# Kernel optimization log

Measured on AMD Instinct MI355X. Metric: run time of the kernel, lower is better.

The kernel has to match this reference:

```python
import jax, jax.numpy as jnp
import numpy as np

EMBED = 768
NH = 12          # num_heads
NL = 3           # num_levels
NP = 4           # num_points
DV = 384         # value dim = embed_dim * deform_ratio(0.5)
DH = DV // NH    # per-head value dim = 32
B = 16
LQ = 1024        # (512/16)^2 ViT tokens
SHAPES = [(64, 64), (32, 32), (16, 16)]  # 1/8, 1/16, 1/32 pyramid of 512x512
LKV = sum(h * w for h, w in SHAPES)      # 5376
EPS = 1e-6


def layer_norm(x, w, b):
    mu = jnp.mean(x, axis=-1, keepdims=True)
    var = jnp.mean((x - mu) ** 2, axis=-1, keepdims=True)
    return (x - mu) / jnp.sqrt(var + EPS) * w + b


def bilinear_sample(v, loc, H, W):
    # v: (B, NH, H*W, DH); loc: (B, Lq, NH, P, 2) normalized in [0,1]
    # Matches torch grid_sample(align_corners=False, padding_mode='zeros').
    Bv, Lq = loc.shape[0], loc.shape[1]
    x = loc[..., 0] * W - 0.5
    y = loc[..., 1] * H - 0.5
    x0 = jnp.floor(x)
    y0 = jnp.floor(y)
    dx = x - x0
    dy = y - y0
    x0i = x0.astype(jnp.int32)
    y0i = y0.astype(jnp.int32)

    def gather(xi, yi):
        valid = (xi >= 0) & (xi < W) & (yi >= 0) & (yi < H)  # (B,Lq,NH,P)
        xc = jnp.clip(xi, 0, W - 1)
        yc = jnp.clip(yi, 0, H - 1)
        lin = (yc * W + xc).transpose(0, 2, 1, 3).reshape(Bv, NH, Lq * NP)
        g = jnp.take_along_axis(v, lin[..., None], axis=2)  # (B,NH,Lq*P,DH)
        g = g.reshape(Bv, NH, Lq, NP, DH).transpose(0, 2, 1, 3, 4)  # (B,Lq,NH,P,DH)
        return g * valid[..., None].astype(g.dtype)

    g00 = gather(x0i, y0i)
    g01 = gather(x0i + 1, y0i)
    g10 = gather(x0i, y0i + 1)
    g11 = gather(x0i + 1, y0i + 1)
    w00 = ((1 - dx) * (1 - dy))[..., None]
    w01 = (dx * (1 - dy))[..., None]
    w10 = ((1 - dx) * dy)[..., None]
    w11 = (dx * dy)[..., None]
    return g00 * w00 + g01 * w01 + g10 * w10 + g11 * w11


def ms_deform_attn_core(value, shapes_list, loc, aw):
    # value: (B,LKV,NH,DH); loc: (B,Lq,NH,NL,NP,2); aw: (B,Lq,NH,NL,NP)
    Bv, Lq = loc.shape[0], loc.shape[1]
    samples = []
    idx = 0
    for l, (H, W) in enumerate(shapes_list):
        v = value[:, idx:idx + H * W].transpose(0, 2, 1, 3)  # (B,NH,HW,DH)
        idx += H * W
        samples.append(bilinear_sample(v, loc[:, :, :, l], H, W))
    s = jnp.stack(samples, axis=3)  # (B,Lq,NH,NL,NP,DH)
    o = jnp.einsum('bqhlp,bqhlpd->bqhd', aw, s)
    return o.reshape(Bv, Lq, NH * DH)


def setup_inputs() -> dict:
    key = jax.random.key(0)
    ks = jax.random.split(key, 12)

    def n(k, shape, s=0.02):
        return jax.random.normal(k, shape, jnp.float32) * s

    return {
        'q': jax.random.normal(ks[0], (B, LQ, EMBED), jnp.float32),
        'reference_points': jax.random.uniform(ks[1], (B, LQ, NL, 2), jnp.float32),
        'kv': jax.random.normal(ks[2], (B, LKV, EMBED), jnp.float32),
        'spatial_shapes': jnp.asarray(SHAPES, jnp.int32),
        'level_start_index': jnp.asarray(
            np.cumsum([0] + [h * w for h, w in SHAPES])[:-1], jnp.int32),
        'ln1_w': jnp.ones(EMBED, jnp.float32),
        'ln1_b': jnp.zeros(EMBED, jnp.float32),
        'ln2_w': jnp.ones(EMBED, jnp.float32),
        'ln2_b': jnp.zeros(EMBED, jnp.float32),
        'gamma': n(ks[3], (EMBED,), 0.1),
        'w_off': n(ks[4], (EMBED, NH * NL * NP * 2)),
        'b_off': n(ks[5], (NH * NL * NP * 2,), 0.01),
        'w_aw': n(ks[6], (EMBED, NH * NL * NP)),
        'b_aw': jnp.zeros(NH * NL * NP, jnp.float32),
        'w_val': n(ks[7], (EMBED, DV)),
        'b_val': jnp.zeros(DV, jnp.float32),
        'w_out': n(ks[8], (DV, EMBED)),
        'b_out': jnp.zeros(EMBED, jnp.float32),
    }


def reference(q, reference_points, kv, spatial_shapes, level_start_index,
              ln1_w, ln1_b, ln2_w, ln2_b, gamma,
              w_off, b_off, w_aw, b_aw, w_val, b_val, w_out, b_out):
    shapes_list = [tuple(int(v) for v in r) for r in np.asarray(spatial_shapes)]
    Bq, Lq, _ = q.shape
    qn = layer_norm(q, ln1_w, ln1_b)
    kvn = layer_norm(kv, ln2_w, ln2_b)
    value = (kvn @ w_val + b_val).reshape(Bq, -1, NH, DH)
    off = (qn @ w_off + b_off).reshape(Bq, Lq, NH, NL, NP, 2)
    aw = (qn @ w_aw + b_aw).reshape(Bq, Lq, NH, NL * NP)
    aw = jax.nn.softmax(aw, axis=-1).reshape(Bq, Lq, NH, NL, NP)
    # offset normalizer is (W_l, H_l) per level
    wh = jnp.asarray([[w, h] for (h, w) in shapes_list], q.dtype)  # (NL,2)
    loc = reference_points[:, :, None, :, None, :] + off / wh[None, None, None, :, None, :]
    attn = ms_deform_attn_core(value, shapes_list, loc, aw)
    attn = attn @ w_out + b_out
    return q + gamma * attn
```

## Files before the change

### kernel.cpp

```cpp
#include <hip/hip_runtime.h>

#define DEV __device__ __forceinline__

typedef short bf16x8 __attribute__((ext_vector_type(8)));
typedef float f32x4 __attribute__((ext_vector_type(4)));
typedef unsigned int u32;
typedef __attribute__((address_space(1))) const u32* gas_ptr;
typedef __attribute__((address_space(3))) u32* las_ptr;

DEV short f2bf(float f) {
  union { float f; unsigned u; } un; un.f = f;
  unsigned r = un.u + 0x7FFFu + ((un.u >> 16) & 1u);
  return (short)(r >> 16);
}
DEV float bf2f(unsigned short s) {
  union { unsigned u; float f; } un;
  un.u = ((unsigned)s) << 16;
  return un.f;
}
DEV void gload16(const short* g, short* l) {
  __builtin_amdgcn_global_load_lds((gas_ptr)g, (las_ptr)l, 16, 0, 0);
}
DEV float hsum4(float4 v) { return v.x + v.y + v.z + v.w; }

__global__ __launch_bounds__(256) void pack_weights_kernel(
    const float* __restrict__ w_val, const float* __restrict__ w_off,
    const float* __restrict__ w_aw, const float* __restrict__ w_out,
    const float* __restrict__ b_off, const float* __restrict__ b_aw,
    short* __restrict__ wT_val, short* __restrict__ wT_offaw,
    short* __restrict__ wT_out, float* __restrict__ bias_cat) {
  int gid = blockIdx.x * 256 + threadIdx.x;
  const int S0 = 768 * 384, S1 = 768 * 288, S2 = 768 * 144, S3 = 384 * 768;
  const int S4 = 80 * 768, S5 = 512;
  if (gid < S0) { int k = gid / 384, n = gid % 384; wT_val[n * 768 + k] = f2bf(w_val[gid]); return; }
  gid -= S0;
  if (gid < S1) { int k = gid / 288, n = gid % 288; wT_offaw[n * 768 + k] = f2bf(w_off[gid]); return; }
  gid -= S1;
  if (gid < S2) { int k = gid / 144, n = gid % 144; wT_offaw[(288 + n) * 768 + k] = f2bf(w_aw[gid]); return; }
  gid -= S2;
  if (gid < S3) { int k = gid / 768, n = gid % 768; wT_out[n * 384 + k] = f2bf(w_out[gid]); return; }
  gid -= S3;
  if (gid < S4) { wT_offaw[432 * 768 + gid] = 0; return; }
  gid -= S4;
  if (gid < S5) { bias_cat[gid] = (gid < 288) ? b_off[gid] : (gid < 432 ? b_aw[gid - 288] : 0.f); }
}

__global__ __launch_bounds__(256) void ln_norm4_kernel(
    const float* __restrict__ x, const float* __restrict__ w,
    const float* __restrict__ b, short* __restrict__ y) {
  const int wv = threadIdx.x >> 6, lane = threadIdx.x & 63;
  const int row = blockIdx.x * 4 + wv;
  const float* xr = x + (size_t)row * 768;
  float4 v0 = *(const float4*)(xr + lane * 4);
  float4 v1 = *(const float4*)(xr + 256 + lane * 4);
  float4 v2 = *(const float4*)(xr + 512 + lane * 4);
  float s = hsum4(v0) + hsum4(v1) + hsum4(v2);
  #pragma unroll
  for (int off = 32; off > 0; off >>= 1) s += __shfl_xor(s, off, 64);
  const float mu = s * (1.f / 768.f);
  float4 d0 = make_float4(v0.x - mu, v0.y - mu, v0.z - mu, v0.w - mu);
  float4 d1 = make_float4(v1.x - mu, v1.y - mu, v1.z - mu, v1.w - mu);
  float4 d2 = make_float4(v2.x - mu, v2.y - mu, v2.z - mu, v2.w - mu);
  float vs = d0.x * d0.x + d0.y * d0.y + d0.z * d0.z + d0.w * d0.w +
             d1.x * d1.x + d1.y * d1.y + d1.z * d1.z + d1.w * d1.w +
             d2.x * d2.x + d2.y * d2.y + d2.z * d2.z + d2.w * d2.w;
  #pragma unroll
  for (int off = 32; off > 0; off >>= 1) vs += __shfl_xor(vs, off, 64);
  const float rs = rsqrtf(vs * (1.f / 768.f) + 1e-6f);
  const float4 w0 = *(const float4*)(w + lane * 4);
  const float4 w1 = *(const float4*)(w + 256 + lane * 4);
  const float4 w2 = *(const float4*)(w + 512 + lane * 4);
  const float4 b0 = *(const float4*)(b + lane * 4);
  const float4 b1 = *(const float4*)(b + 256 + lane * 4);
  const float4 b2 = *(const float4*)(b + 512 + lane * 4);
  unsigned short* yr = (unsigned short*)y + (size_t)row * 768;
  ushort4 o;
  o.x = (unsigned short)f2bf(d0.x * rs * w0.x + b0.x);
  o.y = (unsigned short)f2bf(d0.y * rs * w0.y + b0.y);
  o.z = (unsigned short)f2bf(d0.z * rs * w0.z + b0.z);
  o.w = (unsigned short)f2bf(d0.w * rs * w0.w + b0.w);
  *(ushort4*)(yr + lane * 4) = o;
  o.x = (unsigned short)f2bf(d1.x * rs * w1.x + b1.x);
  o.y = (unsigned short)f2bf(d1.y * rs * w1.y + b1.y);
  o.z = (unsigned short)f2bf(d1.z * rs * w1.z + b1.z);
  o.w = (unsigned short)f2bf(d1.w * rs * w1.w + b1.w);
  *(ushort4*)(yr + 256 + lane * 4) = o;
  o.x = (unsigned short)f2bf(d2.x * rs * w2.x + b2.x);
  o.y = (unsigned short)f2bf(d2.y * rs * w2.y + b2.y);
  o.z = (unsigned short)f2bf(d2.z * rs * w2.z + b2.z);
  o.w = (unsigned short)f2bf(d2.w * rs * w2.w + b2.w);
  *(ushort4*)(yr + 512 + lane * 4) = o;
}

template <int EMODE>
__global__ __launch_bounds__(256, 3) void gemm128_kernel(
    const short* __restrict__ A, const short* __restrict__ Wt,
    const float* __restrict__ bias, const float* __restrict__ qres,
    const float* __restrict__ gamma, void* __restrict__ Cout,
    const int N, const int K) {
  __shared__ __align__(16) short As[128 * 32];
  __shared__ __align__(16) short Bs[128 * 32];
  const int tid = threadIdx.x;
  const int wave = tid >> 6, lane = tid & 63;

  const int nx = gridDim.x;
  const int id = blockIdx.y * nx + blockIdx.x;
  const int cpx = (nx * gridDim.y) >> 3;
  const int swz = (id & 7) * cpx + (id >> 3);
  const int n0 = (swz % nx) * 128, row0 = (swz / nx) * 128;

  const int lr = lane & 15, quad = lane >> 4;
  const int wm = wave >> 1, wn = wave & 1;

  const short* gA[2]; const short* gB[2];
  #pragma unroll
  for (int rnd = 0; rnd < 2; rnd++) {
    int G = rnd * 256 + wave * 64 + lane;
    int line = G >> 3, pos = G & 7, x = pos ^ (line & 7);
    int r = line * 2 + (x >> 2), qk = (x & 3) * 8;
    gA[rnd] = A + (size_t)(row0 + r) * K + qk;
    gB[rnd] = Wt + (size_t)(n0 + r) * K + qk;
  }
  short* ldsA[2] = {&As[(wave * 64) * 8], &As[(256 + wave * 64) * 8]};
  short* ldsB[2] = {&Bs[(wave * 64) * 8], &Bs[(256 + wave * 64) * 8]};

  const short* aF[4]; const short* bF[4];
  #pragma unroll
  for (int t4 = 0; t4 < 4; t4++) {
    int r = wm * 64 + t4 * 16 + lr;
    int line = r >> 1, pos = ((r & 1) * 4 + quad) ^ (line & 7);
    aF[t4] = &As[(line * 8 + pos) * 8];
    int rb = wn * 64 + t4 * 16 + lr;
    int lineb = rb >> 1, posb = ((rb & 1) * 4 + quad) ^ (lineb & 7);
    bF[t4] = &Bs[(lineb * 8 + posb) * 8];
  }

  f32x4 acc[4][4];
  #pragma unroll
  for (int i = 0; i < 4; i++)
    #pragma unroll
    for (int j = 0; j < 4; j++)
      #pragma unroll
      for (int e = 0; e < 4; e++) acc[i][j][e] = 0.f;

  for (int k0 = 0; k0 < K; k0 += 32) {
    gload16(gA[0], ldsA[0]);
    gload16(gA[1], ldsA[1]);
    gload16(gB[0], ldsB[0]);
    gload16(gB[1], ldsB[1]);
    gA[0] += 32; gA[1] += 32; gB[0] += 32; gB[1] += 32;
    __syncthreads();
    bf16x8 av[4], bv[4];
    #pragma unroll
    for (int t4 = 0; t4 < 4; t4++) {
      av[t4] = *(const bf16x8*)aF[t4];
      bv[t4] = *(const bf16x8*)bF[t4];
    }
    #pragma unroll
    for (int ct = 0; ct < 4; ct++)
      #pragma unroll
      for (int rt = 0; rt < 4; rt++)
        acc[rt][ct] = __builtin_amdgcn_mfma_f32_16x16x32_bf16(av[rt], bv[ct], acc[rt][ct], 0, 0, 0);
    __syncthreads();
  }

  #pragma unroll
  for (int ct = 0; ct < 4; ct++) {
    const int n = n0 + wn * 64 + ct * 16 + lr;
    const float bs = bias[n];
    const float gm = (EMODE == 2) ? gamma[n] : 0.f;
    #pragma unroll
    for (int rt = 0; rt < 4; rt++) {
      #pragma unroll
      for (int i = 0; i < 4; i++) {
        const int m = row0 + wm * 64 + rt * 16 + quad * 4 + i;
        float v = acc[rt][ct][i] + bs;
        if (EMODE == 0) {
          ((short*)Cout)[(size_t)m * N + n] = f2bf(v);
        } else if (EMODE == 1) {
          ((float*)Cout)[(size_t)m * N + n] = v;
        } else {
          ((float*)Cout)[(size_t)m * N + n] = qres[(size_t)m * N + n] + gm * v;
        }
      }
    }
  }
}

__global__ __launch_bounds__(384) void sampler_kernel(
    const float* __restrict__ offaw,
    const float* __restrict__ refp,
    const short* __restrict__ value,
    short* __restrict__ o) {
  const int tid = threadIdx.x;
  const int qi = tid / 96, t = tid % 96;
  const int head = t >> 3, ln4 = t & 7;
  const int bq = blockIdx.x * 4 + qi;
  __shared__ __align__(16) float s[4][440];
  __shared__ float sref[4][6];
  const float* row = offaw + (size_t)bq * 512;
  #pragma unroll
  for (int i = t; i < 108; i += 96)
    *(float4*)&s[qi][i * 4] = *(const float4*)&row[i * 4];
  if (t < 6) sref[qi][t] = refp[(size_t)bq * 6 + t];
  __syncthreads();

  const float* awp = &s[qi][288 + head * 12];
  float mx = awp[0];
  #pragma unroll
  for (int j = 1; j < 12; j++) mx = fmaxf(mx, awp[j]);
  float wgt[12];
  float ssum = 0.f;
  #pragma unroll
  for (int j = 0; j < 12; j++) { float e = __expf(awp[j] - mx); wgt[j] = e; ssum += e; }
  const float inv = 1.f / ssum;

  const int b = bq >> 10;
  const unsigned short* vb =
      (const unsigned short*)value + (size_t)b * 5376 * 384 + head * 32 + ln4 * 4;
  float4 acc = make_float4(0.f, 0.f, 0.f, 0.f);
  const int HW[3] = {64, 32, 16};
  const int starts[3] = {0, 4096, 5120};
  #pragma unroll
  for (int l = 0; l < 3; l++) {
    const int Wi = HW[l];
    const float Wf = (float)Wi;
    const float rx = sref[qi][l * 2], ry = sref[qi][l * 2 + 1];
    const unsigned short* base = vb + (size_t)starts[l] * 384;
    #pragma unroll
    for (int p = 0; p < 4; p++) {
      const int oi = ((head * 3 + l) * 4 + p) * 2;
      float x = fmaf(rx, Wf, s[qi][oi] - 0.5f);
      float y = fmaf(ry, Wf, s[qi][oi + 1] - 0.5f);
      float xf = floorf(x), yf = floorf(y);
      float dx = x - xf, dy = y - yf;
      int x0 = (int)xf, y0 = (int)yf;
      int x1 = x0 + 1, y1 = y0 + 1;
      int x0c = min(max(x0, 0), Wi - 1), x1c = min(max(x1, 0), Wi - 1);
      int y0c = min(max(y0, 0), Wi - 1), y1c = min(max(y1, 0), Wi - 1);
      float wx0 = (x0 >= 0 && x0 < Wi) ? (1.f - dx) : 0.f;
      float wx1 = (x1 < Wi && x1 >= 0) ? dx : 0.f;
      float wy0 = (y0 >= 0 && y0 < Wi) ? (1.f - dy) : 0.f;
      float wy1 = (y1 < Wi && y1 >= 0) ? dy : 0.f;
      const ushort4 u00 = *(const ushort4*)(base + (size_t)(y0c * Wi + x0c) * 384);
      const ushort4 u01 = *(const ushort4*)(base + (size_t)(y0c * Wi + x1c) * 384);
      const ushort4 u10 = *(const ushort4*)(base + (size_t)(y1c * Wi + x0c) * 384);
      const ushort4 u11 = *(const ushort4*)(base + (size_t)(y1c * Wi + x1c) * 384);
      const float w00 = wx0 * wy0, w01 = wx1 * wy0, w10 = wx0 * wy1, w11 = wx1 * wy1;
      const float g = wgt[l * 4 + p];
      acc.x += g * (w00 * bf2f(u00.x) + w01 * bf2f(u01.x) + w10 * bf2f(u10.x) + w11 * bf2f(u11.x));
      acc.y += g * (w00 * bf2f(u00.y) + w01 * bf2f(u01.y) + w10 * bf2f(u10.y) + w11 * bf2f(u11.y));
      acc.z += g * (w00 * bf2f(u00.z) + w01 * bf2f(u01.z) + w10 * bf2f(u10.z) + w11 * bf2f(u11.z));
      acc.w += g * (w00 * bf2f(u00.w) + w01 * bf2f(u01.w) + w10 * bf2f(u10.w) + w11 * bf2f(u11.w));
    }
  }
  ushort4 outv;
  outv.x = (unsigned short)f2bf(acc.x * inv);
  outv.y = (unsigned short)f2bf(acc.y * inv);
  outv.z = (unsigned short)f2bf(acc.z * inv);
  outv.w = (unsigned short)f2bf(acc.w * inv);
  *(ushort4*)((unsigned short*)o + (size_t)bq * 384 + head * 32 + ln4 * 4) = outv;
}

extern "C" void kernel_launch(void* const* d_in, const int* in_sizes, int n_in,
                              void* d_out, int out_size, void* d_ws, size_t ws_size,
                              hipStream_t stream) {
  (void)in_sizes; (void)n_in; (void)out_size; (void)ws_size;
  const float* q     = (const float*)d_in[0];
  const float* refp  = (const float*)d_in[1];
  const float* kv    = (const float*)d_in[2];
  const float* ln1w  = (const float*)d_in[5];
  const float* ln1b  = (const float*)d_in[6];
  const float* ln2w  = (const float*)d_in[7];
  const float* ln2b  = (const float*)d_in[8];
  const float* gamma = (const float*)d_in[9];
  const float* w_off = (const float*)d_in[10];
  const float* b_off = (const float*)d_in[11];
  const float* w_aw  = (const float*)d_in[12];
  const float* b_aw  = (const float*)d_in[13];
  const float* w_val = (const float*)d_in[14];
  const float* b_val = (const float*)d_in[15];
  const float* w_out = (const float*)d_in[16];
  const float* b_out = (const float*)d_in[17];
  float* out = (float*)d_out;

  char* wsp = (char*)d_ws;
  size_t cur = 0;
  auto alloc = [&](size_t bytes) -> void* {
    cur = (cur + 255) & ~(size_t)255;
    void* p = wsp + cur;
    cur += bytes;
    return p;
  };
  short*  wT_val   = (short*)alloc((size_t)384 * 768 * 2);
  short*  wT_offaw = (short*)alloc((size_t)512 * 768 * 2);
  short*  wT_out   = (short*)alloc((size_t)768 * 384 * 2);
  float*  bias_cat = (float*)alloc((size_t)512 * 4);
  short*  kvn      = (short*)alloc((size_t)86016 * 768 * 2);
  short*  qn       = (short*)alloc((size_t)16384 * 768 * 2);
  short*  value    = (short*)alloc((size_t)86016 * 384 * 2);
  float*  offaw    = (float*)alloc((size_t)16384 * 512 * 4);
  short*  obuf     = (short*)alloc((size_t)16384 * 384 * 2);

  pack_weights_kernel<<<3842, 256, 0, stream>>>(w_val, w_off, w_aw, w_out, b_off,
                                                b_aw, wT_val, wT_offaw, wT_out,
                                                bias_cat);
  ln_norm4_kernel<<<21504, 256, 0, stream>>>(kv, ln2w, ln2b, kvn);
  ln_norm4_kernel<<<4096, 256, 0, stream>>>(q, ln1w, ln1b, qn);
  gemm128_kernel<0><<<dim3(3, 672), 256, 0, stream>>>(
      kvn, wT_val, b_val, nullptr, nullptr, value, 384, 768);
  gemm128_kernel<1><<<dim3(4, 128), 256, 0, stream>>>(
      qn, wT_offaw, bias_cat, nullptr, nullptr, offaw, 512, 768);
  sampler_kernel<<<4096, 384, 0, stream>>>(offaw, refp, value, obuf);
  gemm128_kernel<2><<<dim3(6, 128), 256, 0, stream>>>(
      obuf, wT_out, b_out, q, gamma, out, 768, 384);
}
```

Before: 665.8 us.

## Fuse prep kernels, merge projection GEMMs, double-buffer GEMM LDS loads

Merges weight packing and both layer norms into one launch, and rewrites weight packing so each thread writes eight contiguous bf16 values. Combines the value and offset/attention-weight GEMMs into a single launch with a swizzled block mapping. Double-buffers the GEMM shared-memory tiles, using manual vmcnt waits so the next tile's global load overlaps the current tile's MFMAs. Also swizzles the sampler's block order. This cuts launch count and load latency at the cost of double the LDS per GEMM block, which may lower occupancy.

```diff
diff --git a/kernel.cpp b/kernel.cpp
--- a/kernel.cpp
+++ b/kernel.cpp
@@ -23,33 +23,11 @@
 }
 DEV float hsum4(float4 v) { return v.x + v.y + v.z + v.w; }
 
-__global__ __launch_bounds__(256) void pack_weights_kernel(
-    const float* __restrict__ w_val, const float* __restrict__ w_off,
-    const float* __restrict__ w_aw, const float* __restrict__ w_out,
-    const float* __restrict__ b_off, const float* __restrict__ b_aw,
-    short* __restrict__ wT_val, short* __restrict__ wT_offaw,
-    short* __restrict__ wT_out, float* __restrict__ bias_cat) {
-  int gid = blockIdx.x * 256 + threadIdx.x;
-  const int S0 = 768 * 384, S1 = 768 * 288, S2 = 768 * 144, S3 = 384 * 768;
-  const int S4 = 80 * 768, S5 = 512;
-  if (gid < S0) { int k = gid / 384, n = gid % 384; wT_val[n * 768 + k] = f2bf(w_val[gid]); return; }
-  gid -= S0;
-  if (gid < S1) { int k = gid / 288, n = gid % 288; wT_offaw[n * 768 + k] = f2bf(w_off[gid]); return; }
-  gid -= S1;
-  if (gid < S2) { int k = gid / 144, n = gid % 144; wT_offaw[(288 + n) * 768 + k] = f2bf(w_aw[gid]); return; }
-  gid -= S2;
-  if (gid < S3) { int k = gid / 768, n = gid % 768; wT_out[n * 384 + k] = f2bf(w_out[gid]); return; }
-  gid -= S3;
-  if (gid < S4) { wT_offaw[432 * 768 + gid] = 0; return; }
-  gid -= S4;
-  if (gid < S5) { bias_cat[gid] = (gid < 288) ? b_off[gid] : (gid < 432 ? b_aw[gid - 288] : 0.f); }
-}
-
-__global__ __launch_bounds__(256) void ln_norm4_kernel(
-    const float* __restrict__ x, const float* __restrict__ w,
-    const float* __restrict__ b, short* __restrict__ y) {
+DEV void ln_row4(const float* __restrict__ x, const float* __restrict__ w,
+                 const float* __restrict__ b, short* __restrict__ y,
+                 const int rb) {
   const int wv = threadIdx.x >> 6, lane = threadIdx.x & 63;
-  const int row = blockIdx.x * 4 + wv;
+  const int row = rb * 4 + wv;
   const float* xr = x + (size_t)row * 768;
   float4 v0 = *(const float4*)(xr + lane * 4);
   float4 v1 = *(const float4*)(xr + 256 + lane * 4);
@@ -92,27 +70,74 @@
   *(ushort4*)(yr + 512 + lane * 4) = o;
 }
 
-template <int EMODE>
-__global__ __launch_bounds__(256, 3) void gemm128_kernel(
-    const short* __restrict__ A, const short* __restrict__ Wt,
-    const float* __restrict__ bias, const float* __restrict__ qres,
-    const float* __restrict__ gamma, void* __restrict__ Cout,
-    const int N, const int K) {
-  __shared__ __align__(16) short As[128 * 32];
-  __shared__ __align__(16) short Bs[128 * 32];
+__global__ __launch_bounds__(256) void fused_pre_kernel(
+    const float* __restrict__ kv, const float* __restrict__ q,
+    const float* __restrict__ ln2w, const float* __restrict__ ln2b,
+    const float* __restrict__ ln1w, const float* __restrict__ ln1b,
+    short* __restrict__ kvn, short* __restrict__ qn,
+    const float* __restrict__ w_val, const float* __restrict__ w_off,
+    const float* __restrict__ w_aw, const float* __restrict__ w_out,
+    const float* __restrict__ b_off, const float* __restrict__ b_aw,
+    short* __restrict__ wT_val, short* __restrict__ wT_offaw,
+    short* __restrict__ wT_out, float* __restrict__ bias_cat) {
+  const int bid = blockIdx.x;
+  if (bid < 21504) { ln_row4(kv, ln2w, ln2b, kvn, bid); return; }
+  if (bid < 25600) { ln_row4(q, ln1w, ln1b, qn, bid - 21504); return; }
+  int g = (bid - 25600) * 256 + threadIdx.x;
+  bf16x8 v;
+  if (g < 36864) {
+    int n = g / 96, k0 = (g % 96) * 8;
+    #pragma unroll
+    for (int i = 0; i < 8; i++) v[i] = f2bf(w_val[(size_t)(k0 + i) * 384 + n]);
+    *(bf16x8*)&wT_val[n * 768 + k0] = v;
+    return;
+  }
+  g -= 36864;
+  if (g < 27648) {
+    int n = g / 96, k0 = (g % 96) * 8;
+    #pragma unroll
+    for (int i = 0; i < 8; i++) v[i] = f2bf(w_off[(size_t)(k0 + i) * 288 + n]);
+    *(bf16x8*)&wT_offaw[n * 768 + k0] = v;
+    return;
+  }
+  g -= 27648;
+  if (g < 13824) {
+    int n = g / 96, k0 = (g % 96) * 8;
+    #pragma unroll
+    for (int i = 0; i < 8; i++) v[i] = f2bf(w_aw[(size_t)(k0 + i) * 144 + n]);
+    *(bf16x8*)&wT_offaw[(288 + n) * 768 + k0] = v;
+    return;
+  }
+  g -= 13824;
+  if (g < 7680) {
+    int n = 432 + g / 96, k0 = (g % 96) * 8;
+    #pragma unroll
+    for (int i = 0; i < 8; i++) v[i] = 0;
+    *(bf16x8*)&wT_offaw[n * 768 + k0] = v;
+    return;
+  }
+  g -= 7680;
+  if (g < 36864) {
+    int n = g / 48, k0 = (g % 48) * 8;
+    #pragma unroll
+    for (int i = 0; i < 8; i++) v[i] = f2bf(w_out[(size_t)(k0 + i) * 768 + n]);
+    *(bf16x8*)&wT_out[n * 384 + k0] = v;
+    return;
+  }
+  g -= 36864;
+  if (g < 512) { bias_cat[g] = (g < 288) ? b_off[g] : (g < 432 ? b_aw[g - 288] : 0.f); }
+}
+
+DEV void gemm_core(const short* __restrict__ A, const short* __restrict__ Wt,
+                   const int K, const int row0, const int n0,
+                   short* As, short* Bs, f32x4 acc[4][4]) {
   const int tid = threadIdx.x;
   const int wave = tid >> 6, lane = tid & 63;
-
-  const int nx = gridDim.x;
-  const int id = blockIdx.y * nx + blockIdx.x;
-  const int cpx = (nx * gridDim.y) >> 3;
-  const int swz = (id & 7) * cpx + (id >> 3);
-  const int n0 = (swz % nx) * 128, row0 = (swz / nx) * 128;
-
   const int lr = lane & 15, quad = lane >> 4;
   const int wm = wave >> 1, wn = wave & 1;
 
   const short* gA[2]; const short* gB[2];
+  int loA[2];
   #pragma unroll
   for (int rnd = 0; rnd < 2; rnd++) {
     int G = rnd * 256 + wave * 64 + lane;
@@ -120,22 +145,20 @@
     int r = line * 2 + (x >> 2), qk = (x & 3) * 8;
     gA[rnd] = A + (size_t)(row0 + r) * K + qk;
     gB[rnd] = Wt + (size_t)(n0 + r) * K + qk;
-  }
-  short* ldsA[2] = {&As[(wave * 64) * 8], &As[(256 + wave * 64) * 8]};
-  short* ldsB[2] = {&Bs[(wave * 64) * 8], &Bs[(256 + wave * 64) * 8]};
-
-  const short* aF[4]; const short* bF[4];
+    loA[rnd] = (rnd * 256 + wave * 64) * 8;
+  }
+
+  int aOff[4], bOff[4];
   #pragma unroll
   for (int t4 = 0; t4 < 4; t4++) {
     int r = wm * 64 + t4 * 16 + lr;
-    int line = r >> 1, pos = ((r & 1) * 4 + quad) ^ (line & 7);
-    aF[t4] = &As[(line * 8 + pos) * 8];
+    int pos = ((r & 1) * 4 + quad) ^ ((r >> 1) & 7);
+    aOff[t4] = ((r >> 1) * 8 + pos) * 8;
     int rb = wn * 64 + t4 * 16 + lr;
-    int lineb = rb >> 1, posb = ((rb & 1) * 4 + quad) ^ (lineb & 7);
-    bF[t4] = &Bs[(lineb * 8 + posb) * 8];
-  }
-
-  f32x4 acc[4][4];
+    int posb = ((rb & 1) * 4 + quad) ^ ((rb >> 1) & 7);
+    bOff[t4] = ((rb >> 1) * 8 + posb) * 8;
+  }
+
   #pragma unroll
   for (int i = 0; i < 4; i++)
     #pragma unroll
@@ -143,45 +166,114 @@
       #pragma unroll
       for (int e = 0; e < 4; e++) acc[i][j][e] = 0.f;
 
-  for (int k0 = 0; k0 < K; k0 += 32) {
-    gload16(gA[0], ldsA[0]);
-    gload16(gA[1], ldsA[1]);
-    gload16(gB[0], ldsB[0]);
-    gload16(gB[1], ldsB[1]);
-    gA[0] += 32; gA[1] += 32; gB[0] += 32; gB[1] += 32;
-    __syncthreads();
+  const int nt = K >> 5;
+  gload16(gA[0], As + loA[0]);
+  gload16(gA[1], As + loA[1]);
+  gload16(gB[0], Bs + loA[0]);
+  gload16(gB[1], Bs + loA[1]);
+  gA[0] += 32; gA[1] += 32; gB[0] += 32; gB[1] += 32;
+
+  int cur = 0;
+  for (int t = 0; t < nt; ++t) {
+    if (t + 1 < nt) {
+      const int nb = (cur ^ 1) * 4096;
+      gload16(gA[0], As + nb + loA[0]);
+      gload16(gA[1], As + nb + loA[1]);
+      gload16(gB[0], Bs + nb + loA[0]);
+      gload16(gB[1], Bs + nb + loA[1]);
+      gA[0] += 32; gA[1] += 32; gB[0] += 32; gB[1] += 32;
+      asm volatile("s_waitcnt vmcnt(4)" ::: "memory");
+    } else {
+      asm volatile("s_waitcnt vmcnt(0)" ::: "memory");
+    }
+    asm volatile("s_barrier" ::: "memory");
+    const int cb = cur * 4096;
     bf16x8 av[4], bv[4];
     #pragma unroll
     for (int t4 = 0; t4 < 4; t4++) {
-      av[t4] = *(const bf16x8*)aF[t4];
-      bv[t4] = *(const bf16x8*)bF[t4];
+      av[t4] = *(const bf16x8*)(As + cb + aOff[t4]);
+      bv[t4] = *(const bf16x8*)(Bs + cb + bOff[t4]);
     }
     #pragma unroll
     for (int ct = 0; ct < 4; ct++)
       #pragma unroll
       for (int rt = 0; rt < 4; rt++)
         acc[rt][ct] = __builtin_amdgcn_mfma_f32_16x16x32_bf16(av[rt], bv[ct], acc[rt][ct], 0, 0, 0);
-    __syncthreads();
-  }
-
+    asm volatile("s_barrier" ::: "memory");
+    cur ^= 1;
+  }
+}
+
+__global__ __launch_bounds__(256, 3) void gemm_dual_kernel(
+    const short* __restrict__ A0, const short* __restrict__ W0,
+    const float* __restrict__ b0, short* __restrict__ C0,
+    const short* __restrict__ A1, const short* __restrict__ W1,
+    const float* __restrict__ b1, float* __restrict__ C1) {
+  __shared__ __align__(16) short As[2 * 128 * 32];
+  __shared__ __align__(16) short Bs[2 * 128 * 32];
+  const int id = blockIdx.x;
+  const int swz = (id & 7) * 316 + (id >> 3);
+  const bool isval = swz < 2016;
+  const short* A; const short* Wt; const float* bias;
+  int row0, n0, N;
+  if (isval) {
+    A = A0; Wt = W0; bias = b0; N = 384;
+    n0 = (swz % 3) * 128; row0 = (swz / 3) * 128;
+  } else {
+    const int o = swz - 2016;
+    A = A1; Wt = W1; bias = b1; N = 512;
+    n0 = (o & 3) * 128; row0 = (o >> 2) * 128;
+  }
+  f32x4 acc[4][4];
+  gemm_core(A, Wt, 768, row0, n0, As, Bs, acc);
+
+  const int lane = threadIdx.x & 63, wave = threadIdx.x >> 6;
+  const int lr = lane & 15, quad = lane >> 4;
+  const int wm = wave >> 1, wn = wave & 1;
   #pragma unroll
   for (int ct = 0; ct < 4; ct++) {
     const int n = n0 + wn * 64 + ct * 16 + lr;
     const float bs = bias[n];
-    const float gm = (EMODE == 2) ? gamma[n] : 0.f;
     #pragma unroll
     for (int rt = 0; rt < 4; rt++) {
       #pragma unroll
       for (int i = 0; i < 4; i++) {
         const int m = row0 + wm * 64 + rt * 16 + quad * 4 + i;
-        float v = acc[rt][ct][i] + bs;
-        if (EMODE == 0) {
-          ((short*)Cout)[(size_t)m * N + n] = f2bf(v);
-        } else if (EMODE == 1) {
-          ((float*)Cout)[(size_t)m * N + n] = v;
-        } else {
-          ((float*)Cout)[(size_t)m * N + n] = qres[(size_t)m * N + n] + gm * v;
-        }
+        const float v = acc[rt][ct][i] + bs;
+        if (isval) C0[(size_t)m * 384 + n] = f2bf(v);
+        else       C1[(size_t)m * 512 + n] = v;
+      }
+    }
+  }
+}
+
+__global__ __launch_bounds__(256, 3) void gemm_final_kernel(
+    const short* __restrict__ A, const short* __restrict__ Wt,
+    const float* __restrict__ bias, const float* __restrict__ qres,
+    const float* __restrict__ gamma, float* __restrict__ Cout) {
+  __shared__ __align__(16) short As[2 * 128 * 32];
+  __shared__ __align__(16) short Bs[2 * 128 * 32];
+  const int id = blockIdx.x;
+  const int swz = (id & 7) * 96 + (id >> 3);
+  const int n0 = (swz % 6) * 128, row0 = (swz / 6) * 128;
+  f32x4 acc[4][4];
+  gemm_core(A, Wt, 384, row0, n0, As, Bs, acc);
+
+  const int lane = threadIdx.x & 63, wave = threadIdx.x >> 6;
+  const int lr = lane & 15, quad = lane >> 4;
+  const int wm = wave >> 1, wn = wave & 1;
+  #pragma unroll
+  for (int ct = 0; ct < 4; ct++) {
+    const int n = n0 + wn * 64 + ct * 16 + lr;
+    const float bs = bias[n];
+    const float gm = gamma[n];
+    #pragma unroll
+    for (int rt = 0; rt < 4; rt++) {
+      #pragma unroll
+      for (int i = 0; i < 4; i++) {
+        const int m = row0 + wm * 64 + rt * 16 + quad * 4 + i;
+        Cout[(size_t)m * 768 + n] =
+            qres[(size_t)m * 768 + n] + gm * (acc[rt][ct][i] + bs);
       }
     }
   }
@@ -195,7 +287,8 @@
   const int tid = threadIdx.x;
   const int qi = tid / 96, t = tid % 96;
   const int head = t >> 3, ln4 = t & 7;
-  const int bq = blockIdx.x * 4 + qi;
+  const int blk = (blockIdx.x & 7) * 512 + (blockIdx.x >> 3);
+  const int bq = blk * 4 + qi;
   __shared__ __align__(16) float s[4][440];
   __shared__ float sref[4][6];
   const float* row = offaw + (size_t)bq * 512;
@@ -302,16 +395,13 @@
   float*  offaw    = (float*)alloc((size_t)16384 * 512 * 4);
   short*  obuf     = (short*)alloc((size_t)16384 * 384 * 2);
 
-  pack_weights_kernel<<<3842, 256, 0, stream>>>(w_val, w_off, w_aw, w_out, b_off,
-                                                b_aw, wT_val, wT_offaw, wT_out,
-                                                bias_cat);
-  ln_norm4_kernel<<<21504, 256, 0, stream>>>(kv, ln2w, ln2b, kvn);
-  ln_norm4_kernel<<<4096, 256, 0, stream>>>(q, ln1w, ln1b, qn);
-  gemm128_kernel<0><<<dim3(3, 672), 256, 0, stream>>>(
-      kvn, wT_val, b_val, nullptr, nullptr, value, 384, 768);
-  gemm128_kernel<1><<<dim3(4, 128), 256, 0, stream>>>(
-      qn, wT_offaw, bias_cat, nullptr, nullptr, offaw, 512, 768);
+  fused_pre_kernel<<<26082, 256, 0, stream>>>(
+      kv, q, ln2w, ln2b, ln1w, ln1b, kvn, qn,
+      w_val, w_off, w_aw, w_out, b_off, b_aw,
+      wT_val, wT_offaw, wT_out, bias_cat);
+  gemm_dual_kernel<<<2528, 256, 0, stream>>>(
+      kvn, wT_val, b_val, value, qn, wT_offaw, bias_cat, offaw);
   sampler_kernel<<<4096, 384, 0, stream>>>(offaw, refp, value, obuf);
-  gemm128_kernel<2><<<dim3(6, 128), 256, 0, stream>>>(
-      obuf, wT_out, b_out, q, gamma, out, 768, 384);
-}
+  gemm_final_kernel<<<768, 256, 0, stream>>>(
+      obuf, wT_out, b_out, q, gamma, out);
+}
```

Result: no change. 655.2 us (-1.6%).
